# Optimization experiments

Measured on AMD Instinct MI355X. Metric: run time of the kernel, lower is better.

The kernel has to match this reference:

```python
import jax, jax.numpy as jnp
import numpy as np

HEAD_SIZE = 64
EMB_SIZE = 1024
B, N = 4, 4096


def setup_inputs() -> dict:
    key = jax.random.key(0)
    kx, kk, kq, kv = jax.random.split(key, 4)
    x = jax.random.normal(kx, (B, N, EMB_SIZE), dtype=jnp.float32)
    # nn.Linear(emb, head, bias=False): weight [head, emb]; y = x @ W.T
    s = 1.0 / np.sqrt(EMB_SIZE)
    Wk = jax.random.uniform(kk, (HEAD_SIZE, EMB_SIZE), jnp.float32, -s, s)
    Wq = jax.random.uniform(kq, (HEAD_SIZE, EMB_SIZE), jnp.float32, -s, s)
    Wv = jax.random.uniform(kv, (HEAD_SIZE, EMB_SIZE), jnp.float32, -s, s)
    return {"x": x, "Wk": Wk, "Wq": Wq, "Wv": Wv}


def reference(x, Wk, Wq, Wv):
    # k, q, v: [B, N, H]
    k = jnp.einsum("bne,he->bnh", x, Wk)
    q = jnp.einsum("bne,he->bnh", x, Wq)
    v = jnp.einsum("bne,he->bnh", x, Wv)
    scale = HEAD_SIZE ** -0.5
    aff = jnp.einsum("bqh,bkh->bqk", q, k) * scale  # [B, N, N]
    aff = jax.nn.softmax(aff, axis=2)
    # dropout rate is 0.0 -> identity
    return jnp.einsum("bqk,bkh->bqh", aff, v)
```

## Files before the change

kernel.cpp:

```cpp
#include <hip/hip_runtime.h>

#define NB   4
#define SEQ  4096
#define EMB  1024
#define HS   64

typedef __attribute__((ext_vector_type(8))) short bf16x8;
typedef __attribute__((ext_vector_type(4))) float f32x4;

__device__ inline unsigned short f2bf(float f) {
  unsigned int u = __float_as_uint(f);
  u += 0x7fffu + ((u >> 16) & 1u);
  return (unsigned short)(u >> 16);
}
__device__ inline float bf2f(unsigned short h) {
  return __uint_as_float(((unsigned int)h) << 16);
}
__device__ inline int swzi64(int row, int c) {
  return row * 64 + ((c ^ (row & 7)) << 3);
}
__device__ inline int swzi32(int row, int c) {
  return row * 32 + ((c ^ ((row >> 1) & 3)) << 3);
}
__device__ inline int swzi128(int row, int c) {
  return row * 128 + ((c ^ (row & 7)) << 3);
}
__device__ inline void gld16(const unsigned short* g, unsigned short* l) {
  __builtin_amdgcn_global_load_lds(
      (const __attribute__((address_space(1))) void*)g,
      (__attribute__((address_space(3))) void*)l, 16, 0, 0);
}

__global__ __launch_bounds__(256) void wprep(
    const float* __restrict__ Wk, const float* __restrict__ Wq,
    const float* __restrict__ Wv,
    unsigned short* __restrict__ Wh, unsigned short* __restrict__ Wl) {
  int i = blockIdx.x * 256 + threadIdx.x;
  int e = i >> 8, c = i & 255;
  float4 v;
  float sc = 1.0f;
  if (e < 64)       { v = ((const float4*)Wq)[e * 256 + c];
                      sc = 0.18033688011112042f; }
  else if (e < 128)   v = ((const float4*)Wk)[(e - 64) * 256 + c];
  else                v = ((const float4*)Wv)[(e - 128) * 256 + c];
  v.x *= sc; v.y *= sc; v.z *= sc; v.w *= sc;
  ushort4 hv, lv;
  hv.x = f2bf(v.x); lv.x = f2bf(v.x - bf2f(hv.x));
  hv.y = f2bf(v.y); lv.y = f2bf(v.y - bf2f(hv.y));
  hv.z = f2bf(v.z); lv.z = f2bf(v.z - bf2f(hv.z));
  hv.w = f2bf(v.w); lv.w = f2bf(v.w - bf2f(hv.w));
  *(ushort4*)&Wh[i * 4] = hv;
  *(ushort4*)&Wl[i * 4] = lv;
}

#define XhSp(p) ((unsigned short*)(SM + (p) * 2048))
#define XlSp(p) ((unsigned short*)(SM + 4096 + (p) * 2048))

__global__ __launch_bounds__(256, 2) void qkv_x1(
    const float* __restrict__ x,
    const unsigned short* __restrict__ Wh, const unsigned short* __restrict__ Wl,
    unsigned short* __restrict__ qh, unsigned short* __restrict__ ql,
    unsigned short* __restrict__ kh, unsigned short* __restrict__ kl,
    unsigned short* __restrict__ vt) {
  __shared__ __align__(16) unsigned char SM[8192];

  const int t  = threadIdx.x;
  const int l  = t & 63;
  const int li = l & 15;
  const int g  = l >> 4;
  const int w  = t >> 6;
  const int m0 = blockIdx.x * 32;
  const int b  = m0 >> 12;
  const int n0 = m0 & 4095;

  const int xrow = t >> 3;
  const float* xp = x + (m0 + xrow) * EMB + (t & 7) * 4;
  const int xaddr = xrow * 32 + ((((t & 7) >> 1) ^ ((xrow >> 1) & 3)) << 3)
                    + (t & 1) * 4;

  const int r0 = 48 * w + li, r1 = r0 + 16, r2 = r0 + 32;
  const unsigned short* const Wh0 = Wh + r0 * EMB + 8 * g;
  const unsigned short* const Wh1 = Wh + r1 * EMB + 8 * g;
  const unsigned short* const Wh2 = Wh + r2 * EMB + 8 * g;
  const unsigned short* const Wl0 = Wl + r0 * EMB + 8 * g;
  const unsigned short* const Wl1 = Wl + r1 * EMB + 8 * g;
  const unsigned short* const Wl2 = Wl + r2 * EMB + 8 * g;

  f32x4 acc[2][3];
#pragma unroll
  for (int i = 0; i < 2; ++i)
#pragma unroll
    for (int j = 0; j < 3; ++j) acc[i][j] = (f32x4){0.f, 0.f, 0.f, 0.f};

  const int rA0 = li, rA1 = 16 + li;

  auto loadB = [&](int s, bf16x8 (&B)[6]) {
    const int ko = s * 32;
    B[0] = *(const bf16x8*)&Wh0[ko];
    B[1] = *(const bf16x8*)&Wh1[ko];
    B[2] = *(const bf16x8*)&Wh2[ko];
    B[3] = *(const bf16x8*)&Wl0[ko];
    B[4] = *(const bf16x8*)&Wl1[ko];
    B[5] = *(const bf16x8*)&Wl2[ko];
  };
  auto writeX = [&](float4 v, int p) {
    unsigned short h0 = f2bf(v.x), h1 = f2bf(v.y), h2 = f2bf(v.z), h3 = f2bf(v.w);
    unsigned short e0 = f2bf(v.x - bf2f(h0)), e1 = f2bf(v.y - bf2f(h1));
    unsigned short e2 = f2bf(v.z - bf2f(h2)), e3 = f2bf(v.w - bf2f(h3));
    int2 hv, lv;
    hv.x = (int)((unsigned)h0 | ((unsigned)h1 << 16));
    hv.y = (int)((unsigned)h2 | ((unsigned)h3 << 16));
    lv.x = (int)((unsigned)e0 | ((unsigned)e1 << 16));
    lv.y = (int)((unsigned)e2 | ((unsigned)e3 << 16));
    *(int2*)&XhSp(p)[xaddr] = hv;
    *(int2*)&XlSp(p)[xaddr] = lv;
  };

  bf16x8 B0[6], B1[6];
  loadB(0, B0);
  writeX(*(const float4*)xp, 0);
  float4 pxA = *(const float4*)(xp + 32);
  float4 pxB = *(const float4*)(xp + 64);
  __syncthreads();

  auto step = [&](int s, bf16x8 (&Bc)[6], bf16x8 (&Bn)[6]) {
    const int p = s & 1;
    if (s < 31) loadB(s + 1, Bn);

    bf16x8 ah0 = *(const bf16x8*)&XhSp(p)[swzi32(rA0, g)];
    bf16x8 ah1 = *(const bf16x8*)&XhSp(p)[swzi32(rA1, g)];
    bf16x8 al0 = *(const bf16x8*)&XlSp(p)[swzi32(rA0, g)];
    bf16x8 al1 = *(const bf16x8*)&XlSp(p)[swzi32(rA1, g)];

    __builtin_amdgcn_s_setprio(1);
    acc[0][0] = __builtin_amdgcn_mfma_f32_16x16x32_bf16(ah0, Bc[0], acc[0][0], 0,0,0);
    acc[0][0] = __builtin_amdgcn_mfma_f32_16x16x32_bf16(ah0, Bc[3], acc[0][0], 0,0,0);
    acc[0][0] = __builtin_amdgcn_mfma_f32_16x16x32_bf16(al0, Bc[0], acc[0][0], 0,0,0);
    acc[0][1] = __builtin_amdgcn_mfma_f32_16x16x32_bf16(ah0, Bc[1], acc[0][1], 0,0,0);
    acc[0][1] = __builtin_amdgcn_mfma_f32_16x16x32_bf16(ah0, Bc[4], acc[0][1], 0,0,0);
    acc[0][1] = __builtin_amdgcn_mfma_f32_16x16x32_bf16(al0, Bc[1], acc[0][1], 0,0,0);
    acc[0][2] = __builtin_amdgcn_mfma_f32_16x16x32_bf16(ah0, Bc[2], acc[0][2], 0,0,0);
    acc[0][2] = __builtin_amdgcn_mfma_f32_16x16x32_bf16(ah0, Bc[5], acc[0][2], 0,0,0);
    acc[0][2] = __builtin_amdgcn_mfma_f32_16x16x32_bf16(al0, Bc[2], acc[0][2], 0,0,0);
    acc[1][0] = __builtin_amdgcn_mfma_f32_16x16x32_bf16(ah1, Bc[0], acc[1][0], 0,0,0);
    acc[1][0] = __builtin_amdgcn_mfma_f32_16x16x32_bf16(ah1, Bc[3], acc[1][0], 0,0,0);
    acc[1][0] = __builtin_amdgcn_mfma_f32_16x16x32_bf16(al1, Bc[0], acc[1][0], 0,0,0);
    acc[1][1] = __builtin_amdgcn_mfma_f32_16x16x32_bf16(ah1, Bc[1], acc[1][1], 0,0,0);
    acc[1][1] = __builtin_amdgcn_mfma_f32_16x16x32_bf16(ah1, Bc[4], acc[1][1], 0,0,0);
    acc[1][1] = __builtin_amdgcn_mfma_f32_16x16x32_bf16(al1, Bc[1], acc[1][1], 0,0,0);
    acc[1][2] = __builtin_amdgcn_mfma_f32_16x16x32_bf16(ah1, Bc[2], acc[1][2], 0,0,0);
    acc[1][2] = __builtin_amdgcn_mfma_f32_16x16x32_bf16(ah1, Bc[5], acc[1][2], 0,0,0);
    acc[1][2] = __builtin_amdgcn_mfma_f32_16x16x32_bf16(al1, Bc[2], acc[1][2], 0,0,0);
    __builtin_amdgcn_s_setprio(0);

    if (s < 31) {
      writeX(pxA, p ^ 1);
      pxA = pxB;
      if (s < 29) pxB = *(const float4*)(xp + (s + 3) * 32);
    }

    asm volatile("s_waitcnt lgkmcnt(0)" ::: "memory");
    __builtin_amdgcn_s_barrier();
    __builtin_amdgcn_sched_barrier(0);
  };

  for (int s2 = 0; s2 < 16; ++s2) {
    step(2 * s2,     B0, B1);
    step(2 * s2 + 1, B1, B0);
  }

#pragma unroll
  for (int i = 0; i < 2; ++i)
#pragma unroll
    for (int j = 0; j < 3; ++j) {
      const int H3 = 48 * w + 16 * j + li;
#pragma unroll
      for (int r = 0; r < 4; ++r) {
        const int mrow = 16 * i + 4 * g + r;
        const float vv = acc[i][j][r];
        if (H3 < 64) {
          const unsigned short hb = f2bf(vv);
          const int off = (b * SEQ + n0 + mrow) * HS + H3;
          qh[off] = hb; ql[off] = f2bf(vv - bf2f(hb));
        } else if (H3 < 128) {
          const unsigned short hb = f2bf(vv);
          const int off = (b * SEQ + n0 + mrow) * HS + (H3 - 64);
          kh[off] = hb; kl[off] = f2bf(vv - bf2f(hb));
        } else {
          vt[(b * HS + (H3 - 128)) * SEQ + n0 + mrow] = f2bf(vv);
        }
      }
    }
}

__global__ __launch_bounds__(512) void attn_mfma(
    const unsigned short* __restrict__ qh, const unsigned short* __restrict__ ql,
    const unsigned short* __restrict__ kh, const unsigned short* __restrict__ kl,
    const unsigned short* __restrict__ vt, float* __restrict__ out) {
  __shared__ __align__(16) unsigned char SM[118784];
  unsigned short* const PtS = (unsigned short*)(SM + 98304);

  const int t  = threadIdx.x;
  const int l  = t & 63;
  const int li = l & 15;
  const int g  = l >> 4;
  const int w  = t >> 6;
  const int qg = w & 1;
  const int ks = w >> 1;
  const int b  = blockIdx.y;
  const int q0 = blockIdx.x << 6;

  bf16x8 qfh[2][2], qfl[2][2];
#pragma unroll
  for (int qs = 0; qs < 2; ++qs) {
    const unsigned short* qrh = qh + (b * SEQ + q0 + 32 * qg + 16 * qs + li) * HS;
    const unsigned short* qrl = ql + (b * SEQ + q0 + 32 * qg + 16 * qs + li) * HS;
    qfh[qs][0] = *(const bf16x8*)&qrh[8 * g];
    qfh[qs][1] = *(const bf16x8*)&qrh[32 + 8 * g];
    qfl[qs][0] = *(const bf16x8*)&qrl[8 * g];
    qfl[qs][1] = *(const bf16x8*)&qrl[32 + 8 * g];
  }

  const int kconst = (l >> 3) * HS + (((l & 7) ^ (l >> 3)) << 3);
  const int rowl = l >> 4, slot = l & 15;
  const int vcE = rowl * SEQ + ((slot ^ rowl) << 3);
  const int vcO = rowl * SEQ + ((slot ^ (4 + rowl)) << 3);
  const unsigned short* khB = kh + b * SEQ * HS;
  const unsigned short* klB = kl + b * SEQ * HS;
  const unsigned short* vtB = vt + b * HS * SEQ;
  const int sA = 2 * w, sB = 2 * w + 1;

  f32x4 O[4][2];
#pragma unroll
  for (int ht = 0; ht < 4; ++ht) {
    O[ht][0] = (f32x4){0.f, 0.f, 0.f, 0.f};
    O[ht][1] = (f32x4){0.f, 0.f, 0.f, 0.f};
  }
  float lp0 = 0.f, lp1 = 0.f;
  unsigned short* const PtW = PtS + w * 1280;

  auto stage = [&](int it, int p) {
    const int kt0 = it << 7;
    unsigned short* const KhP = (unsigned short*)(SM + p * 16384);
    unsigned short* const KlP = (unsigned short*)(SM + 32768 + p * 16384);
    unsigned short* const VtP = (unsigned short*)(SM + 65536 + p * 16384);
    gld16(khB + (kt0 + 8 * sA) * HS + kconst, KhP + sA * 512);
    gld16(khB + (kt0 + 8 * sB) * HS + kconst, KhP + sB * 512);
    gld16(klB + (kt0 + 8 * sA) * HS + kconst, KlP + sA * 512);
    gld16(klB + (kt0 + 8 * sB) * HS + kconst, KlP + sB * 512);
    gld16(vtB + 4 * sA * SEQ + kt0 + vcE, VtP + sA * 512);
    gld16(vtB + 4 * sB * SEQ + kt0 + vcO, VtP + sB * 512);
  };

  stage(0, 0);
  __syncthreads();

  for (int it = 0; it < 32; ++it) {
    const int p = it & 1;
    if (it < 31) stage(it + 1, p ^ 1);

    unsigned short* const KhS = (unsigned short*)(SM + p * 16384);
    unsigned short* const KlS = (unsigned short*)(SM + 32768 + p * 16384);
    unsigned short* const VtS = (unsigned short*)(SM + 65536 + p * 16384);

    f32x4 S[2][2];
    S[0][0] = (f32x4){-32.f, -32.f, -32.f, -32.f};
    S[0][1] = (f32x4){-32.f, -32.f, -32.f, -32.f};
    S[1][0] = (f32x4){-32.f, -32.f, -32.f, -32.f};
    S[1][1] = (f32x4){-32.f, -32.f, -32.f, -32.f};
    __builtin_amdgcn_s_setprio(1);
#pragma unroll
    for (int khf = 0; khf < 2; ++khf) {
      const int cc = 4 * khf + g;
#pragma unroll
      for (int kt = 0; kt < 2; ++kt) {
        const int row = 32 * ks + 16 * kt + li;
        bf16x8 akh = *(const bf16x8*)&KhS[swzi64(row, cc)];
        bf16x8 akl = *(const bf16x8*)&KlS[swzi64(row, cc)];
        S[kt][0] = __builtin_amdgcn_mfma_f32_16x16x32_bf16(akh, qfh[0][khf], S[kt][0], 0,0,0);
        S[kt][0] = __builtin_amdgcn_mfma_f32_16x16x32_bf16(akh, qfl[0][khf], S[kt][0], 0,0,0);
        S[kt][0] = __builtin_amdgcn_mfma_f32_16x16x32_bf16(akl, qfh[0][khf], S[kt][0], 0,0,0);
        S[kt][1] = __builtin_amdgcn_mfma_f32_16x16x32_bf16(akh, qfh[1][khf], S[kt][1], 0,0,0);
        S[kt][1] = __builtin_amdgcn_mfma_f32_16x16x32_bf16(akh, qfl[1][khf], S[kt][1], 0,0,0);
        S[kt][1] = __builtin_amdgcn_mfma_f32_16x16x32_bf16(akl, qfh[1][khf], S[kt][1], 0,0,0);
      }
    }
    __builtin_amdgcn_s_setprio(0);

#pragma unroll
    for (int kt = 0; kt < 2; ++kt)
#pragma unroll
      for (int qs = 0; qs < 2; ++qs) {
        unsigned pu[4];
        float ls = 0.f;
#pragma unroll
        for (int r = 0; r < 4; ++r) {
          const float pe = exp2f(S[kt][qs][r]);
          pu[r] = __float_as_uint(pe);
          ls += __uint_as_float(pu[r] & 0xffff0000u);
        }
        if (qs == 0) lp0 += ls; else lp1 += ls;
        const unsigned p01 = __builtin_amdgcn_perm(pu[1], pu[0], 0x07060302u);
        const unsigned p23 = __builtin_amdgcn_perm(pu[3], pu[2], 0x07060302u);
        const int qrow = 16 * qs + li;
        const int c = 2 * kt + (g >> 1);
        const int addr = qrow * 40 + (((c ^ (qrow & 3))) << 3) + ((g & 1) << 2);
        int2 pv; pv.x = (int)p01; pv.y = (int)p23;
        *(int2*)&PtW[addr] = pv;
      }

    asm volatile("" ::: "memory");

    bf16x8 pb0 = *(const bf16x8*)&PtW[li * 40 + ((g ^ (li & 3)) << 3)];
    {
      const int r1 = 16 + li;
      bf16x8 pb1 = *(const bf16x8*)&PtW[r1 * 40 + ((g ^ (r1 & 3)) << 3)];
      __builtin_amdgcn_s_setprio(1);
#pragma unroll
      for (int ht = 0; ht < 4; ++ht) {
        const int vrow = 16 * ht + li;
        bf16x8 va = *(const bf16x8*)&VtS[swzi128(vrow, 4 * ks + g)];
        O[ht][0] = __builtin_amdgcn_mfma_f32_16x16x32_bf16(va, pb0, O[ht][0], 0,0,0);
        O[ht][1] = __builtin_amdgcn_mfma_f32_16x16x32_bf16(va, pb1, O[ht][1], 0,0,0);
      }
      __builtin_amdgcn_s_setprio(0);
    }

    __syncthreads();
  }


  lp0 += __shfl_xor(lp0, 16); lp0 += __shfl_xor(lp0, 32);
  lp1 += __shfl_xor(lp1, 16); lp1 += __shfl_xor(lp1, 32);

  float* const OTm = (float*)SM;
  float* const Lm  = (float*)(SM + 65536);
#pragma unroll
  for (int ht = 0; ht < 4; ++ht)
#pragma unroll
    for (int qs = 0; qs < 2; ++qs) {
      float4 o4;
      o4.x = O[ht][qs][0]; o4.y = O[ht][qs][1];
      o4.z = O[ht][qs][2]; o4.w = O[ht][qs][3];
      *(float4*)&OTm[w * 2048 + (16 * qs + li) * 64 + 16 * ht + 4 * g] = o4;
    }
  if (g == 0) { Lm[w * 32 + li] = lp0; Lm[w * 32 + 16 + li] = lp1; }
  __syncthreads();

  {
    const int q = t >> 3, h8 = (t & 7) << 3;
    const int qq = q & 31, qgf = q >> 5;
    float lF = 0.f;
    float4 a = {0.f, 0.f, 0.f, 0.f}, c4 = {0.f, 0.f, 0.f, 0.f};
#pragma unroll
    for (int k2 = 0; k2 < 4; ++k2) {
      const int ww = qgf + 2 * k2;
      lF += Lm[ww * 32 + qq];
      const float* Ob = OTm + ww * 2048 + qq * 64 + h8;
      float4 u = *(const float4*)Ob;
      float4 v = *(const float4*)(Ob + 4);
      a.x += u.x; a.y += u.y; a.z += u.z; a.w += u.w;
      c4.x += v.x; c4.y += v.y; c4.z += v.z; c4.w += v.w;
    }
    const float inv = 1.f / lF;
    a.x *= inv; a.y *= inv; a.z *= inv; a.w *= inv;
    c4.x *= inv; c4.y *= inv; c4.z *= inv; c4.w *= inv;
    float* op = out + (b * SEQ + q0 + q) * HS + h8;
    *(float4*)op = a;
    *(float4*)(op + 4) = c4;
  }
}

extern "C" void kernel_launch(void* const* d_in, const int* in_sizes, int n_in,
                              void* d_out, int out_size, void* d_ws,
                              size_t ws_size, hipStream_t stream) {
  const float* x  = (const float*)d_in[0];
  const float* Wk = (const float*)d_in[1];
  const float* Wq = (const float*)d_in[2];
  const float* Wv = (const float*)d_in[3];
  float* out = (float*)d_out;

  unsigned short* us = (unsigned short*)d_ws;
  unsigned short* qh = us + 0 * (1 << 20);
  unsigned short* ql = us + 1 * (1 << 20);
  unsigned short* kh = us + 2 * (1 << 20);
  unsigned short* kl = us + 3 * (1 << 20);
  unsigned short* vt = us + 4 * (1 << 20);
  unsigned short* Wh = us + 5 * (1 << 20);
  unsigned short* Wl = Wh + 192 * 1024;

  wprep<<<192, 256, 0, stream>>>(Wk, Wq, Wv, Wh, Wl);
  qkv_x1<<<512, 256, 0, stream>>>(x, Wh, Wl, qh, ql, kh, kl, vt);
  attn_mfma<<<dim3(64, NB), 512, 0, stream>>>(qh, ql, kh, kl, vt, out);
}
```

Baseline: 197.8 us.

## Load x directly into registers in QKV projection, removing LDS staging and barriers

The QKV projection kernel no longer stages x through shared memory with double buffering and per-step barriers. Each lane now loads its own fp32 x fragment straight from global memory, converts it to bf16 hi/lo in registers, and feeds the MFMAs, with a two-deep register prefetch of both x and the weights. This removes LDS writes and reads and the block-wide synchronisation. In exchange each x element is loaded by all four waves (redundant global traffic, mostly served from cache), the split conversion is repeated per wave, and register pressure rises, with the occupancy hint of 2 blocks per CU dropped from the launch bounds.

```diff
diff --git a/kernel.cpp b/kernel.cpp
--- a/kernel.cpp
+++ b/kernel.cpp
@@ -18,9 +18,6 @@
 }
 __device__ inline int swzi64(int row, int c) {
   return row * 64 + ((c ^ (row & 7)) << 3);
-}
-__device__ inline int swzi32(int row, int c) {
-  return row * 32 + ((c ^ ((row >> 1) & 3)) << 3);
 }
 __device__ inline int swzi128(int row, int c) {
   return row * 128 + ((c ^ (row & 7)) << 3);
@@ -53,17 +50,15 @@
   *(ushort4*)&Wl[i * 4] = lv;
 }
 
-#define XhSp(p) ((unsigned short*)(SM + (p) * 2048))
-#define XlSp(p) ((unsigned short*)(SM + 4096 + (p) * 2048))
-
-__global__ __launch_bounds__(256, 2) void qkv_x1(
+struct Araw { float4 x0, x1, y0, y1; };
+struct Bfr  { bf16x8 h0, h1, h2, l0, l1, l2; };
+
+__global__ __launch_bounds__(256) void qkv_x1(
     const float* __restrict__ x,
     const unsigned short* __restrict__ Wh, const unsigned short* __restrict__ Wl,
     unsigned short* __restrict__ qh, unsigned short* __restrict__ ql,
     unsigned short* __restrict__ kh, unsigned short* __restrict__ kl,
     unsigned short* __restrict__ vt) {
-  __shared__ __align__(16) unsigned char SM[8192];
-
   const int t  = threadIdx.x;
   const int l  = t & 63;
   const int li = l & 15;
@@ -73,10 +68,8 @@
   const int b  = m0 >> 12;
   const int n0 = m0 & 4095;
 
-  const int xrow = t >> 3;
-  const float* xp = x + (m0 + xrow) * EMB + (t & 7) * 4;
-  const int xaddr = xrow * 32 + ((((t & 7) >> 1) ^ ((xrow >> 1) & 3)) << 3)
-                    + (t & 1) * 4;
+  const float* const xr0 = x + (m0 + li) * EMB + 8 * g;
+  const float* const xr1 = x + (m0 + 16 + li) * EMB + 8 * g;
 
   const int r0 = 48 * w + li, r1 = r0 + 16, r2 = r0 + 32;
   const unsigned short* const Wh0 = Wh + r0 * EMB + 8 * g;
@@ -92,81 +85,72 @@
 #pragma unroll
     for (int j = 0; j < 3; ++j) acc[i][j] = (f32x4){0.f, 0.f, 0.f, 0.f};
 
-  const int rA0 = li, rA1 = 16 + li;
-
-  auto loadB = [&](int s, bf16x8 (&B)[6]) {
+  auto loadA = [&](int s) {
+    Araw A;
     const int ko = s * 32;
-    B[0] = *(const bf16x8*)&Wh0[ko];
-    B[1] = *(const bf16x8*)&Wh1[ko];
-    B[2] = *(const bf16x8*)&Wh2[ko];
-    B[3] = *(const bf16x8*)&Wl0[ko];
-    B[4] = *(const bf16x8*)&Wl1[ko];
-    B[5] = *(const bf16x8*)&Wl2[ko];
-  };
-  auto writeX = [&](float4 v, int p) {
-    unsigned short h0 = f2bf(v.x), h1 = f2bf(v.y), h2 = f2bf(v.z), h3 = f2bf(v.w);
-    unsigned short e0 = f2bf(v.x - bf2f(h0)), e1 = f2bf(v.y - bf2f(h1));
-    unsigned short e2 = f2bf(v.z - bf2f(h2)), e3 = f2bf(v.w - bf2f(h3));
-    int2 hv, lv;
-    hv.x = (int)((unsigned)h0 | ((unsigned)h1 << 16));
-    hv.y = (int)((unsigned)h2 | ((unsigned)h3 << 16));
-    lv.x = (int)((unsigned)e0 | ((unsigned)e1 << 16));
-    lv.y = (int)((unsigned)e2 | ((unsigned)e3 << 16));
-    *(int2*)&XhSp(p)[xaddr] = hv;
-    *(int2*)&XlSp(p)[xaddr] = lv;
-  };
-
-  bf16x8 B0[6], B1[6];
-  loadB(0, B0);
-  writeX(*(const float4*)xp, 0);
-  float4 pxA = *(const float4*)(xp + 32);
-  float4 pxB = *(const float4*)(xp + 64);
-  __syncthreads();
-
-  auto step = [&](int s, bf16x8 (&Bc)[6], bf16x8 (&Bn)[6]) {
-    const int p = s & 1;
-    if (s < 31) loadB(s + 1, Bn);
-
-    bf16x8 ah0 = *(const bf16x8*)&XhSp(p)[swzi32(rA0, g)];
-    bf16x8 ah1 = *(const bf16x8*)&XhSp(p)[swzi32(rA1, g)];
-    bf16x8 al0 = *(const bf16x8*)&XlSp(p)[swzi32(rA0, g)];
-    bf16x8 al1 = *(const bf16x8*)&XlSp(p)[swzi32(rA1, g)];
-
+    A.x0 = *(const float4*)(xr0 + ko);
+    A.x1 = *(const float4*)(xr0 + ko + 4);
+    A.y0 = *(const float4*)(xr1 + ko);
+    A.y1 = *(const float4*)(xr1 + ko + 4);
+    return A;
+  };
+  auto loadB = [&](int s) {
+    Bfr B;
+    const int ko = s * 32;
+    B.h0 = *(const bf16x8*)&Wh0[ko];
+    B.h1 = *(const bf16x8*)&Wh1[ko];
+    B.h2 = *(const bf16x8*)&Wh2[ko];
+    B.l0 = *(const bf16x8*)&Wl0[ko];
+    B.l1 = *(const bf16x8*)&Wl1[ko];
+    B.l2 = *(const bf16x8*)&Wl2[ko];
+    return B;
+  };
+  auto cvtpair = [&](const float4& u, const float4& v, bf16x8& hi, bf16x8& lo) {
+    const unsigned short h0 = f2bf(u.x), h1 = f2bf(u.y);
+    const unsigned short h2 = f2bf(u.z), h3 = f2bf(u.w);
+    const unsigned short h4 = f2bf(v.x), h5 = f2bf(v.y);
+    const unsigned short h6 = f2bf(v.z), h7 = f2bf(v.w);
+    hi = (bf16x8){(short)h0, (short)h1, (short)h2, (short)h3,
+                  (short)h4, (short)h5, (short)h6, (short)h7};
+    lo = (bf16x8){(short)f2bf(u.x - bf2f(h0)), (short)f2bf(u.y - bf2f(h1)),
+                  (short)f2bf(u.z - bf2f(h2)), (short)f2bf(u.w - bf2f(h3)),
+                  (short)f2bf(v.x - bf2f(h4)), (short)f2bf(v.y - bf2f(h5)),
+                  (short)f2bf(v.z - bf2f(h6)), (short)f2bf(v.w - bf2f(h7))};
+  };
+  auto compute = [&](const Araw& A, const Bfr& B) {
+    bf16x8 ah0, al0, ah1, al1;
+    cvtpair(A.x0, A.x1, ah0, al0);
+    cvtpair(A.y0, A.y1, ah1, al1);
     __builtin_amdgcn_s_setprio(1);
-    acc[0][0] = __builtin_amdgcn_mfma_f32_16x16x32_bf16(ah0, Bc[0], acc[0][0], 0,0,0);
-    acc[0][0] = __builtin_amdgcn_mfma_f32_16x16x32_bf16(ah0, Bc[3], acc[0][0], 0,0,0);
-    acc[0][0] = __builtin_amdgcn_mfma_f32_16x16x32_bf16(al0, Bc[0], acc[0][0], 0,0,0);
-    acc[0][1] = __builtin_amdgcn_mfma_f32_16x16x32_bf16(ah0, Bc[1], acc[0][1], 0,0,0);
-    acc[0][1] = __builtin_amdgcn_mfma_f32_16x16x32_bf16(ah0, Bc[4], acc[0][1], 0,0,0);
-    acc[0][1] = __builtin_amdgcn_mfma_f32_16x16x32_bf16(al0, Bc[1], acc[0][1], 0,0,0);
-    acc[0][2] = __builtin_amdgcn_mfma_f32_16x16x32_bf16(ah0, Bc[2], acc[0][2], 0,0,0);
-    acc[0][2] = __builtin_amdgcn_mfma_f32_16x16x32_bf16(ah0, Bc[5], acc[0][2], 0,0,0);
-    acc[0][2] = __builtin_amdgcn_mfma_f32_16x16x32_bf16(al0, Bc[2], acc[0][2], 0,0,0);
-    acc[1][0] = __builtin_amdgcn_mfma_f32_16x16x32_bf16(ah1, Bc[0], acc[1][0], 0,0,0);
-    acc[1][0] = __builtin_amdgcn_mfma_f32_16x16x32_bf16(ah1, Bc[3], acc[1][0], 0,0,0);
-    acc[1][0] = __builtin_amdgcn_mfma_f32_16x16x32_bf16(al1, Bc[0], acc[1][0], 0,0,0);
-    acc[1][1] = __builtin_amdgcn_mfma_f32_16x16x32_bf16(ah1, Bc[1], acc[1][1], 0,0,0);
-    acc[1][1] = __builtin_amdgcn_mfma_f32_16x16x32_bf16(ah1, Bc[4], acc[1][1], 0,0,0);
-    acc[1][1] = __builtin_amdgcn_mfma_f32_16x16x32_bf16(al1, Bc[1], acc[1][1], 0,0,0);
-    acc[1][2] = __builtin_amdgcn_mfma_f32_16x16x32_bf16(ah1, Bc[2], acc[1][2], 0,0,0);
-    acc[1][2] = __builtin_amdgcn_mfma_f32_16x16x32_bf16(ah1, Bc[5], acc[1][2], 0,0,0);
-    acc[1][2] = __builtin_amdgcn_mfma_f32_16x16x32_bf16(al1, Bc[2], acc[1][2], 0,0,0);
+    acc[0][0] = __builtin_amdgcn_mfma_f32_16x16x32_bf16(ah0, B.h0, acc[0][0], 0,0,0);
+    acc[0][0] = __builtin_amdgcn_mfma_f32_16x16x32_bf16(ah0, B.l0, acc[0][0], 0,0,0);
+    acc[0][0] = __builtin_amdgcn_mfma_f32_16x16x32_bf16(al0, B.h0, acc[0][0], 0,0,0);
+    acc[0][1] = __builtin_amdgcn_mfma_f32_16x16x32_bf16(ah0, B.h1, acc[0][1], 0,0,0);
+    acc[0][1] = __builtin_amdgcn_mfma_f32_16x16x32_bf16(ah0, B.l1, acc[0][1], 0,0,0);
+    acc[0][1] = __builtin_amdgcn_mfma_f32_16x16x32_bf16(al0, B.h1, acc[0][1], 0,0,0);
+    acc[0][2] = __builtin_amdgcn_mfma_f32_16x16x32_bf16(ah0, B.h2, acc[0][2], 0,0,0);
+    acc[0][2] = __builtin_amdgcn_mfma_f32_16x16x32_bf16(ah0, B.l2, acc[0][2], 0,0,0);
+    acc[0][2] = __builtin_amdgcn_mfma_f32_16x16x32_bf16(al0, B.h2, acc[0][2], 0,0,0);
+    acc[1][0] = __builtin_amdgcn_mfma_f32_16x16x32_bf16(ah1, B.h0, acc[1][0], 0,0,0);
+    acc[1][0] = __builtin_amdgcn_mfma_f32_16x16x32_bf16(ah1, B.l0, acc[1][0], 0,0,0);
+    acc[1][0] = __builtin_amdgcn_mfma_f32_16x16x32_bf16(al1, B.h0, acc[1][0], 0,0,0);
+    acc[1][1] = __builtin_amdgcn_mfma_f32_16x16x32_bf16(ah1, B.h1, acc[1][1], 0,0,0);
+    acc[1][1] = __builtin_amdgcn_mfma_f32_16x16x32_bf16(ah1, B.l1, acc[1][1], 0,0,0);
+    acc[1][1] = __builtin_amdgcn_mfma_f32_16x16x32_bf16(al1, B.h1, acc[1][1], 0,0,0);
+    acc[1][2] = __builtin_amdgcn_mfma_f32_16x16x32_bf16(ah1, B.h2, acc[1][2], 0,0,0);
+    acc[1][2] = __builtin_amdgcn_mfma_f32_16x16x32_bf16(ah1, B.l2, acc[1][2], 0,0,0);
+    acc[1][2] = __builtin_amdgcn_mfma_f32_16x16x32_bf16(al1, B.h2, acc[1][2], 0,0,0);
     __builtin_amdgcn_s_setprio(0);
-
-    if (s < 31) {
-      writeX(pxA, p ^ 1);
-      pxA = pxB;
-      if (s < 29) pxB = *(const float4*)(xp + (s + 3) * 32);
-    }
-
-    asm volatile("s_waitcnt lgkmcnt(0)" ::: "memory");
-    __builtin_amdgcn_s_barrier();
-    __builtin_amdgcn_sched_barrier(0);
-  };
-
+  };
+
+  Araw Aa = loadA(0), Ab;
+  Bfr  Ba = loadB(0), Bb;
   for (int s2 = 0; s2 < 16; ++s2) {
-    step(2 * s2,     B0, B1);
-    step(2 * s2 + 1, B1, B0);
+    const int s = 2 * s2;
+    if (s < 31) { Ab = loadA(s + 1); Bb = loadB(s + 1); }
+    compute(Aa, Ba);
+    if (s + 1 < 31) { Aa = loadA(s + 2); Ba = loadB(s + 2); }
+    compute(Ab, Bb);
   }
 
 #pragma unroll
```

After: 217.4 us. +9.9%, slower.
